# Kernel tuning notes

Measured on AMD Instinct MI355X. Metric: run time of the kernel, lower is better.

## Reference

```python
import jax, jax.numpy as jnp
import numpy as np
import math

D_MODEL = 1024
N_HEADS = 16
HEAD_DIM = D_MODEL // N_HEADS
TEMP = 0.1          # sinkhorn temperature
SINK_ITERS = 10     # update_permutation uses n_iterations=10
EPS = 1e-10


def setup_inputs() -> dict:
    key = jax.random.key(0)
    ks = jax.random.split(key, 16)
    b, n, d = 2, 2048, D_MODEL
    x_data = jax.random.normal(ks[0], (b, n, d), dtype=jnp.float32)
    certainty = jax.random.uniform(ks[1], (b, n), dtype=jnp.float32)
    permutation = jnp.stack([jax.random.permutation(jax.random.fold_in(ks[2], i), n)
                             for i in range(b)]).astype(jnp.int64)
    def lin(k):
        kw, kb = jax.random.split(k)
        W = jax.random.normal(kw, (d, d), dtype=jnp.float32) * 0.02
        bvec = jax.random.normal(kb, (d,), dtype=jnp.float32) * 0.02
        return W, bvec
    Wq, bq = lin(ks[3]); Wk, bk = lin(ks[4]); Wv, bv = lin(ks[5]); Wo, bo = lin(ks[6])
    perm_bias_scale = jnp.ones((1, N_HEADS, 1, 1), dtype=jnp.float32)
    certainty_temp = jnp.ones((1,), dtype=jnp.float32) * 2.0
    return {"x_data": x_data, "certainty": certainty, "permutation": permutation,
            "Wq": Wq, "bq": bq, "Wk": Wk, "bk": bk, "Wv": Wv, "bv": bv,
            "Wo": Wo, "bo": bo, "perm_bias_scale": perm_bias_scale,
            "certainty_temp": certainty_temp}


def reference(x_data, certainty, permutation, Wq, bq, Wk, bk, Wv, bv, Wo, bo,
              perm_bias_scale, certainty_temp):
    b, n, d = x_data.shape
    scale = math.sqrt(HEAD_DIM)

    def proj(W, bias):  # nn.Linear: x @ W.T + b, then split heads -> (b,H,n,hd)
        y = jnp.einsum('bnd,ed->bne', x_data, W) + bias
        return y.reshape(b, n, N_HEADS, HEAD_DIM).transpose(0, 2, 1, 3)

    Q, K, V = proj(Wq, bq), proj(Wk, bk), proj(Wv, bv)

    scores = jnp.einsum('bhnk,bhmk->bhnm', Q, K) / scale  # (b,H,n,n)
    # permutation-distance bias: B[i,j] = -|sigma(i)-sigma(j)| * |scale_h|
    pf = permutation.astype(jnp.float32)
    dist = jnp.abs(pf[:, :, None] - pf[:, None, :])       # (b,n,n)
    scores = scores - dist[:, None, :, :] * jnp.abs(perm_bias_scale)

    attention = jax.nn.softmax(scores, axis=-1)           # dropout is identity (eval)
    out = jnp.einsum('bhnm,bhmd->bhnd', attention, V)
    out = out.transpose(0, 2, 1, 3).reshape(b, n, d)
    output = jnp.einsum('bnd,ed->bne', out, Wo) + bo

    # certainty update from attention entropy
    ent = -(attention * jnp.log(attention + EPS)).sum(-1).mean(1)  # (b,n)
    cert_upd = jax.nn.sigmoid(certainty_temp * (math.log(n) - ent))
    new_certainty = jnp.maximum(certainty, cert_upd)

    # permutation update via Sinkhorn on log mean attention
    avg_attn = attention.mean(axis=1)
    P = jnp.exp(jnp.log(avg_attn + EPS) / TEMP)
    def body(_, P):
        P = P / (P.sum(-1, keepdims=True) + EPS)
        P = P / (P.sum(-2, keepdims=True) + EPS)
        return P
    P = jax.lax.fori_loop(0, SINK_ITERS, body, P)
    idx = jnp.argmax(P, axis=-1)                          # (b,n)
    new_permutation = jnp.take_along_axis(permutation, idx, axis=1)

    return output, new_certainty, new_permutation
```

## Files before the change

### kernel.cpp

```cpp
#include <hip/hip_runtime.h>
#include <cstdint>

#define NTOK 2048
#define DMODEL 1024
#define NHEADS 16
#define HD 64
#define BATCH 2
#define EPSF 1e-10f
#define EPSD 1e-10

typedef __attribute__((ext_vector_type(8))) short bf16x8;
typedef __attribute__((ext_vector_type(8))) _Float16 f16x8;
typedef __attribute__((ext_vector_type(4))) float f32x4;

__device__ __forceinline__ float bf2f(unsigned short u){
  union { unsigned int i; float f; } c; c.i = ((unsigned int)u) << 16; return c.f;
}
__device__ __forceinline__ unsigned short f2bf(float f){
  union { float f; unsigned int u; } c; c.f = f;
  unsigned int u = c.u;
  unsigned int r = (u + 0x7FFFu + ((u >> 16) & 1u)) >> 16;
  return (unsigned short)r;
}
__device__ __forceinline__ unsigned short f2h(float f){
  union { _Float16 h; unsigned short u; } c; c.h = (_Float16)f; return c.u;
}
__device__ __forceinline__ float h2f(unsigned short u){
  union { unsigned short u; _Float16 h; } c; c.u = u; return (float)c.h;
}

__device__ __forceinline__ void async16(const unsigned short* g, unsigned short* lds_base){
  __builtin_amdgcn_global_load_lds((const __attribute__((address_space(1))) unsigned int*)g,
                                   (__attribute__((address_space(3))) unsigned int*)lds_base,
                                   16, 0, 0);
}

template<int BM, int BN>
__device__ __forceinline__ void gemm_bt_core(
    const unsigned short* A, int lda,
    const unsigned short* B, int ldb,
    int K,
    f32x4 (&acc)[BM/32][BN/32],
    unsigned short* ldsA, unsigned short* ldsB)
{
  constexpr int TM = BM/32, TN = BN/32;
  const int tid  = threadIdx.x;
  const int lane = tid & 63;
  const int wave = tid >> 6;
  const int wm = wave >> 1, wn = wave & 1;
  const int fr = lane & 15;
  const int fk = (lane >> 4) << 3;
  const int sr = lane >> 2;
  const int sk = (lane & 3) << 3;

  for (int k0 = 0; k0 < K; k0 += 32){
    #pragma unroll
    for (int c = 0; c < BM/64; c++){
      int ch = c*4 + wave;
      async16(A + (long)(ch*16 + sr)*lda + (k0 + sk), ldsA + ch*512);
    }
    #pragma unroll
    for (int c = 0; c < BN/64; c++){
      int ch = c*4 + wave;
      async16(B + (long)(ch*16 + sr)*ldb + (k0 + sk), ldsB + ch*512);
    }
    __syncthreads();
    bf16x8 af[TM], bf[TN];
    #pragma unroll
    for (int i=0;i<TM;i++)
      af[i] = *(const bf16x8*)(ldsA + ((wm*TM*16) + i*16 + fr)*32 + fk);
    #pragma unroll
    for (int j=0;j<TN;j++)
      bf[j] = *(const bf16x8*)(ldsB + ((wn*TN*16) + j*16 + fr)*32 + fk);
    #pragma unroll
    for (int i=0;i<TM;i++)
      #pragma unroll
      for (int j=0;j<TN;j++)
        acc[i][j] = __builtin_amdgcn_mfma_f32_16x16x32_bf16(af[i], bf[j], acc[i][j], 0, 0, 0);
    __syncthreads();
  }
}

__device__ __forceinline__ double wred_sumd(double x){
  for(int o=32;o;o>>=1) x+=__shfl_xor(x,o); return x;
}


__global__ void f2b_multi(const float* __restrict__ x,
    const float* __restrict__ wq, const float* __restrict__ wk,
    const float* __restrict__ wv, const float* __restrict__ wo,
    unsigned short* __restrict__ out)
{
  int i = blockIdx.x*256 + threadIdx.x;
  int base = i << 2;
  const float* src;
  if (base < 4194304) src = x + base;
  else {
    int d = base - 4194304;
    int r = d >> 20, off = d & 1048575;
    src = (r==0 ? wq : (r==1 ? wk : (r==2 ? wv : wo))) + off;
  }
  float4 v = *(const float4*)src;
  ushort4 o;
  o.x = f2bf(v.x); o.y = f2bf(v.y); o.z = f2bf(v.z); o.w = f2bf(v.w);
  *(ushort4*)(out + base) = o;
}

__global__ void init_kernel(double* __restrict__ uv){
  int idx = blockIdx.x*256 + threadIdx.x;
  if (idx < 8192) uv[idx] = 1.0;
}

__global__ __launch_bounds__(256) void qkv_kernel(
    const unsigned short* __restrict__ xb,
    const unsigned short* __restrict__ Wqb, const float* __restrict__ bq,
    const unsigned short* __restrict__ Wkb, const float* __restrict__ bk,
    const unsigned short* __restrict__ Wvb, const float* __restrict__ bv,
    unsigned short* __restrict__ Qb, unsigned short* __restrict__ Kb,
    unsigned short* __restrict__ Vb)
{
  __shared__ unsigned short lds[(128+128)*32];
  int sel = blockIdx.y >> 3;
  int n0 = (blockIdx.y & 7) * 128;
  int m0 = blockIdx.x * 128;
  const unsigned short* W = sel==0 ? Wqb : (sel==1 ? Wkb : Wvb);
  const float* bias       = sel==0 ? bq  : (sel==1 ? bk  : bv);
  unsigned short* out     = sel==0 ? Qb  : (sel==1 ? Kb  : Vb);
  f32x4 acc[4][4];
  f32x4 z = {0.f,0.f,0.f,0.f};
  for (int i=0;i<4;i++) for(int j=0;j<4;j++) acc[i][j] = z;
  gemm_bt_core<128,128>(xb + (long)m0*DMODEL, DMODEL, W + (long)n0*DMODEL, DMODEL,
                        DMODEL, acc, lds, lds + 128*32);
  int lane = threadIdx.x & 63, wave = threadIdx.x >> 6;
  int wm = wave>>1, wn = wave&1;
  int cr = (lane>>4)<<2, cc = lane & 15;
  for (int i=0;i<4;i++) for(int j=0;j<4;j++) for(int r=0;r<4;r++){
    int row = m0 + wm*64 + i*16 + cr + r;
    int col = n0 + wn*64 + j*16 + cc;
    out[(long)row*DMODEL + col] = f2bf(acc[i][j][r] + bias[col]);
  }
}

__global__ void vtrans_kernel(const unsigned short* __restrict__ Vb,
                              unsigned short* __restrict__ Vt)
{
  __shared__ unsigned short t[32][33];
  int b = blockIdx.z, i0 = blockIdx.x*32, e0 = blockIdx.y*32;
  int tx = threadIdx.x, ty = threadIdx.y;
  for (int r=0;r<32;r+=8) t[ty+r][tx] = Vb[((long)b*NTOK + i0+ty+r)*DMODEL + e0+tx];
  __syncthreads();
  for (int r=0;r<32;r+=8)
    Vt[((long)b*DMODEL + e0+ty+r)*NTOK + i0+tx] = f2h(bf2f(t[tx][ty+r]));
}

__global__ __launch_bounds__(512,4) void attnA_kernel(
    const unsigned short* __restrict__ Qb, const unsigned short* __restrict__ Kb,
    const unsigned short* __restrict__ Vt, const int* __restrict__ perm,
    const float* __restrict__ psc,
    float* __restrict__ mpart, float* __restrict__ lpart, float* __restrict__ Tpart,
    unsigned short* __restrict__ Opart)
{
  __shared__ unsigned short Kt[2*128*32];
  __shared__ unsigned short Vtl[64*136];
  __shared__ unsigned short Pt[128*136];
  __shared__ unsigned short pbs[2048];

  const int tid  = threadIdx.x;
  const int lane = tid & 63;
  const int wave = tid >> 6;
  const int fr   = lane & 15;
  const int fkg  = lane >> 4;
  const int fk   = fkg << 3;
  const int cr   = fkg << 2;
  const int rw   = wave << 4;
  const int rt   = blockIdx.x >> 1;
  const int half = blockIdx.x & 1;
  const int m0   = rt * 128;
  const int h    = blockIdx.y;
  const int b    = blockIdx.z;

  for (int i = tid; i < 2048; i += 512) pbs[i] = (unsigned short)perm[b*NTOK + i];

  bf16x8 qf[2];
  #pragma unroll
  for (int kc=0;kc<2;kc++)
    qf[kc] = *(const bf16x8*)(Qb + ((long)(b*NTOK + m0 + rw + fr))*DMODEL + h*HD + kc*32 + fk);

  const float asc = fabsf(psc[h]);
  __syncthreads();

  float prow[4];
  #pragma unroll
  for (int r=0;r<4;r++) prow[r] = (float)pbs[m0 + rw + cr + r];

  float mrow[4], lrow[4], Trow[4];
  #pragma unroll
  for (int r=0;r<4;r++){ mrow[r] = -1e30f; lrow[r] = 0.f; Trow[r] = 0.f; }
  f32x4 oacc[4];
  {
    f32x4 z = {0.f,0.f,0.f,0.f};
    for (int jj=0;jj<4;jj++) oacc[jj]=z;
  }

  for (int j2=0;j2<8;j2++){
    int j = half*8 + j2;
    __syncthreads();
    #pragma unroll
    for (int c=0;c<2;c++){
      int q = c*8 + wave;
      int kc = q >> 3, rb = (q & 7) * 16;
      async16(Kb + ((long)(b*NTOK + j*128 + rb + (lane>>2)))*DMODEL + h*HD + kc*32 + ((lane&3)<<3),
              Kt + kc*4096 + rb*32);
    }
    {
      int c = tid>>3, sg = tid&7;
      const unsigned short* vg = Vt + ((long)(b*DMODEL + h*HD + c))*NTOK + j*128 + sg*16;
      unsigned short* vl = Vtl + c*136 + sg*16;
      *(uint4*)(vl)   = *(const uint4*)(vg);
      *(uint4*)(vl+8) = *(const uint4*)(vg+8);
    }
    __syncthreads();

    f32x4 sacc[8];
    {
      f32x4 z = {0.f,0.f,0.f,0.f};
      for (int jj=0;jj<8;jj++) sacc[jj]=z;
    }
    #pragma unroll
    for (int kc=0;kc<2;kc++){
      bf16x8 bfr[8];
      #pragma unroll
      for (int jj=0;jj<8;jj++) bfr[jj] = *(const bf16x8*)(Kt + kc*4096 + (jj*16+fr)*32 + fk);
      #pragma unroll
      for (int jj=0;jj<8;jj++)
        sacc[jj] = __builtin_amdgcn_mfma_f32_16x16x32_bf16(qf[kc], bfr[jj], sacc[jj],0,0,0);
    }

    float pcol[8];
    #pragma unroll
    for (int jj=0;jj<8;jj++) pcol[jj] = (float)pbs[j*128 + jj*16 + fr];

    #pragma unroll
    for (int r=0;r<4;r++){
      float sv[8];
      float tm = -1e30f;
      #pragma unroll
      for (int jj=0;jj<8;jj++){
        sv[jj] = sacc[jj][r]*0.125f - fabsf(prow[r]-pcol[jj])*asc;
        tm = fmaxf(tm, sv[jj]);
      }
      #pragma unroll
      for (int o=1;o<16;o<<=1) tm = fmaxf(tm, __shfl_xor(tm,o));
      float nm = fmaxf(mrow[r], tm);
      float alpha = __expf(mrow[r] - nm);
      float lres = lrow[r]*alpha;
      Trow[r] = Trow[r]*alpha + (mrow[r]-nm)*lres;
      #pragma unroll
      for (int jc=0;jc<4;jc++) oacc[jc][r] *= alpha;
      float ts=0.f, tT=0.f;
      int prowbase = (rw + cr + r)*136;
      #pragma unroll
      for (int jj=0;jj<8;jj++){
        float d = sv[jj]-nm;
        float ev = __expf(d);
        ts += ev; tT += ev*d;
        Pt[prowbase + jj*16 + fr] = f2h(ev);
      }
      #pragma unroll
      for (int o=1;o<16;o<<=1){ ts += __shfl_xor(ts,o); tT += __shfl_xor(tT,o); }
      lrow[r] = lres + ts;
      Trow[r] += tT;
      mrow[r] = nm;
    }
    __syncthreads();
    #pragma unroll
    for (int kp=0;kp<4;kp++){
      f16x8 paf, pbf[4];
      paf = *(const f16x8*)(Pt + (rw+fr)*136 + kp*32 + fk);
      #pragma unroll
      for (int jj=0;jj<4;jj++) pbf[jj] = *(const f16x8*)(Vtl + (jj*16+fr)*136 + kp*32 + fk);
      #pragma unroll
      for (int jj=0;jj<4;jj++)
        oacc[jj] = __builtin_amdgcn_mfma_f32_16x16x32_f16(paf, pbf[jj], oacc[jj],0,0,0);
    }
  }

  long pbase = ((long)(half*BATCH + b)*NHEADS + h)*NTOK;
  #pragma unroll
  for (int jj=0;jj<4;jj++)
    #pragma unroll
    for (int r=0;r<4;r++){
      int row = m0 + rw + cr + r;
      Opart[(pbase + row)*HD + jj*16 + fr] = f2bf(oacc[jj][r]);
    }
  if (fr == 0){
    #pragma unroll
    for (int r=0;r<4;r++){
      int row = m0 + rw + cr + r;
      mpart[pbase + row] = mrow[r];
      lpart[pbase + row] = lrow[r];
      Tpart[pbase + row] = Trow[r];
    }
  }
}

__global__ __launch_bounds__(256) void merge_kernel(
    const float* __restrict__ mpart, const float* __restrict__ lpart,
    const float* __restrict__ Tpart, const unsigned short* __restrict__ Opart,
    unsigned short* __restrict__ Ob, float* __restrict__ mbuf,
    float* __restrict__ ilbuf, float* __restrict__ entb)
{
  int tid = threadIdx.x;
  int row = blockIdx.x*4 + (tid>>6);
  int h = blockIdx.y;
  int b = blockIdx.z;
  int col = tid & 63;
  long o1 = ((long)(0*BATCH + b)*NHEADS + h)*NTOK + row;
  long o2 = ((long)(1*BATCH + b)*NHEADS + h)*NTOK + row;
  float m1 = mpart[o1], m2 = mpart[o2];
  float l1 = lpart[o1], l2 = lpart[o2];
  float m = fmaxf(m1, m2);
  float e1 = __expf(m1-m), e2 = __expf(m2-m);
  float l = l1*e1 + l2*e2;
  float il = 1.0f/l;
  float Ov = (bf2f(Opart[o1*HD + col])*e1 + bf2f(Opart[o2*HD + col])*e2)*il;
  Ob[((long)(b*NTOK + row))*DMODEL + h*HD + col] = f2bf(Ov);
  if (col == 0){
    float T = e1*(Tpart[o1] + (m1-m)*l1) + e2*(Tpart[o2] + (m2-m)*l2);
    long off = ((long)(b*NHEADS+h))*NTOK + row;
    mbuf[off] = m; ilbuf[off] = il;
    entb[off] = T*il - __logf(l);
  }
}

__global__ __launch_bounds__(512,4) void avgP_kernel(
    const unsigned short* __restrict__ Qb, const unsigned short* __restrict__ Kb,
    const int* __restrict__ perm, const float* __restrict__ psc,
    const float* __restrict__ mbuf, const float* __restrict__ ilbuf,
    float* __restrict__ avg, unsigned short* __restrict__ avgH,
    unsigned short* __restrict__ avgT)
{
  __shared__ unsigned short Kt[2][8192];
  __shared__ float sm[NHEADS*64];
  __shared__ float si[NHEADS*64];
  __shared__ float sasc[NHEADS];

  const int bid = blockIdx.x;
  const int xcd = bid & 7, idx = bid >> 3;
  const int b   = xcd >> 2;
  const int qy  = (xcd >> 1) & 1, qx = xcd & 1;
  const int ydim = qy*16 + (idx >> 3);
  const int xdim = qx*8  + (idx & 7);
  const int m0   = ydim * 64;
  const int colb = xdim * 128;

  const int tid  = threadIdx.x;
  const int lane = tid & 63;
  const int wave = tid >> 6;
  const int wr = wave >> 2, wc = wave & 3;
  const int rw = wr*32, cb = wc*32;
  const int fr = lane & 15;
  const int fk = (lane >> 4) << 3;
  const int cr = (lane >> 4) << 2;
  const int cc = lane & 15;
  const int sr = lane >> 2;
  const int sk = (lane & 3) << 3;

  const unsigned short* kgp[2];
  int ldsoff[2];
  #pragma unroll
  for (int q=0;q<2;q++){
    int cid = q*8 + wave;
    int kc = cid >> 3, ch = cid & 7;
    kgp[q] = Kb + ((long)(b*NTOK + colb + ch*16 + sr))*DMODEL + kc*32 + sk;
    ldsoff[q] = kc*4096 + ch*512;
  }

  for (int e = tid; e < NHEADS*64; e += 512){
    int h = e >> 6, r = e & 63;
    long off = ((long)(b*NHEADS + h))*NTOK + m0 + r;
    sm[e] = mbuf[off];
    si[e] = ilbuf[off];
  }
  if (tid < NHEADS) sasc[tid] = fabsf(psc[tid]);

  float prw[8];
  #pragma unroll
  for (int i=0;i<2;i++)
    #pragma unroll
    for (int r=0;r<4;r++)
      prw[i*4+r] = (float)perm[b*NTOK + m0 + rw + i*16 + cr + r];
  float pcl[2];
  #pragma unroll
  for (int j=0;j<2;j++)
    pcl[j] = (float)perm[b*NTOK + colb + cb + j*16 + cc];

  const unsigned short* qp[2];
  #pragma unroll
  for (int i=0;i<2;i++)
    qp[i] = Qb + ((long)(b*NTOK + m0 + rw + i*16 + fr))*DMODEL + fk;

  float aacc[2][2][4];
  #pragma unroll
  for (int i=0;i<2;i++) for (int j=0;j<2;j++) for (int r=0;r<4;r++) aacc[i][j][r]=0.f;

  #pragma unroll
  for (int q=0;q<2;q++) async16(kgp[q], &Kt[0][0] + ldsoff[q]);
  __syncthreads();

  unsigned short* curb = &Kt[0][0];
  unsigned short* nxtb = &Kt[1][0];

  #pragma unroll 2
  for (int h=0; h<NHEADS; h++){
    if (h < NHEADS-1){
      #pragma unroll
      for (int q=0;q<2;q++) async16(kgp[q] + (h+1)*HD, nxtb + ldsoff[q]);
    }
    bf16x8 qf[2][2];
    #pragma unroll
    for (int i=0;i<2;i++)
      #pragma unroll
      for (int kc=0;kc<2;kc++)
        qf[i][kc] = *(const bf16x8*)(qp[i] + h*HD + kc*32);

    f32x4 acc[2][2];
    {
      f32x4 z = {0.f,0.f,0.f,0.f};
      acc[0][0]=z; acc[0][1]=z; acc[1][0]=z; acc[1][1]=z;
    }
    #pragma unroll
    for (int kc=0;kc<2;kc++){
      bf16x8 bfr[2];
      #pragma unroll
      for (int j=0;j<2;j++)
        bfr[j] = *(const bf16x8*)(curb + kc*4096 + ((cb>>4) + j)*512 + fr*32 + fk);
      #pragma unroll
      for (int i=0;i<2;i++)
        #pragma unroll
        for (int j=0;j<2;j++)
          acc[i][j] = __builtin_amdgcn_mfma_f32_16x16x32_bf16(qf[i][kc], bfr[j], acc[i][j],0,0,0);
    }
    const float asc = sasc[h];
    #pragma unroll
    for (int i=0;i<2;i++)
      #pragma unroll
      for (int r=0;r<4;r++){
        int rl = rw + i*16 + cr + r;
        float mh = sm[h*64 + rl];
        float ih = si[h*64 + rl];
        #pragma unroll
        for (int j=0;j<2;j++){
          float sv = acc[i][j][r]*0.125f - fabsf(prw[i*4+r]-pcl[j])*asc;
          aacc[i][j][r] += __expf(sv - mh) * ih;
        }
      }
    __syncthreads();
    unsigned short* t = curb; curb = nxtb; nxtb = t;
  }

  unsigned short* T = &Kt[0][0];
  #pragma unroll
  for (int i=0;i<2;i++)
    #pragma unroll
    for (int j=0;j<2;j++)
      #pragma unroll
      for (int r=0;r<4;r++){
        float pw = __expf(__logf(aacc[i][j][r]*0.0625f + EPSF)*10.0f);
        int rl = rw + i*16 + cr + r;
        int cl = cb + j*16 + cc;
        long off = ((long)(b*NTOK + m0 + rl))*NTOK + colb + cl;
        avg[off] = pw;
        unsigned short hv = f2h(pw);
        avgH[off] = hv;
        T[cl*72 + rl] = hv;
      }
  __syncthreads();
  {
    int c = tid >> 2, sg = tid & 3;
    uint4* dst = (uint4*)(avgT + ((long)(b*NTOK + colb + c))*NTOK + m0 + sg*16);
    const unsigned short* src = T + c*72 + sg*16;
    dst[0] = *(const uint4*)(src);
    dst[1] = *(const uint4*)(src + 8);
  }
}

__global__ __launch_bounds__(256) void sink_phase_h(const unsigned short* __restrict__ M,
    const double* __restrict__ x, double* __restrict__ y)
{
  int b = blockIdx.y, tid = threadIdx.x;
  int wave = tid >> 6, lane = tid & 63;
  int i = blockIdx.x*4 + wave;
  const unsigned short* row = M + ((long)b*NTOK + i)*NTOK;
  const double* xb = x + b*NTOK;
  double s = 0.0;
  #pragma unroll
  for (int k=0;k<4;k++){
    int j = k*512 + lane*8;
    f16x8 mv = *(const f16x8*)(row + j);
    #pragma unroll
    for (int e=0;e<8;e++) s += (double)(float)mv[e] * xb[j+e];
  }
  s = wred_sumd(s);
  if (lane == 0){
    double yi = y[b*NTOK + i];
    y[b*NTOK + i] = yi / (yi*s + EPSD);
  }
}

__global__ __launch_bounds__(256) void argmax_kernel(const float* __restrict__ P,
    const double* __restrict__ v, const int* __restrict__ perm,
    float* __restrict__ dout_perm)
{
  int b = blockIdx.y, tid = threadIdx.x;
  int wave = tid >> 6, lane = tid & 63;
  int i = blockIdx.x*4 + wave;
  const float* row = P + ((long)b*NTOK + i)*NTOK;
  const double* vb = v + b*NTOK;
  double bv = -1.0; int bj = 0;
  #pragma unroll
  for (int k=0;k<4;k++){
    int j0 = k*512 + lane*8;
    float4 r0 = *(const float4*)(row + j0);
    float4 r1 = *(const float4*)(row + j0 + 4);
    float rv[8] = {r0.x,r0.y,r0.z,r0.w,r1.x,r1.y,r1.z,r1.w};
    #pragma unroll
    for (int e=0;e<8;e++){
      double val = (double)rv[e]*vb[j0+e];
      if (val>bv){ bv=val; bj=j0+e; }
    }
  }
  for (int o=32;o;o>>=1){
    double ov=__shfl_xor(bv,o); int oj=__shfl_xor(bj,o);
    if (ov>bv || (ov==bv && oj<bj)){bv=ov;bj=oj;}
  }
  if (lane == 0)
    dout_perm[b*NTOK + i] = (float)perm[b*NTOK + bj];
}

__global__ __launch_bounds__(256) void out_kernel(
    const unsigned short* __restrict__ Ob, const unsigned short* __restrict__ Wob,
    const float* __restrict__ bo, float* __restrict__ dout)
{
  __shared__ unsigned short lds[(128+128)*32];
  int m0 = blockIdx.x*128, n0 = blockIdx.y*128;
  f32x4 acc[4][4];
  f32x4 z = {0.f,0.f,0.f,0.f};
  for (int i=0;i<4;i++) for(int j=0;j<4;j++) acc[i][j] = z;
  gemm_bt_core<128,128>(Ob + (long)m0*DMODEL, DMODEL, Wob + (long)n0*DMODEL, DMODEL,
                        DMODEL, acc, lds, lds + 128*32);
  int lane = threadIdx.x & 63, wave = threadIdx.x >> 6;
  int wm = wave>>1, wn = wave&1;
  int cr = (lane>>4)<<2, cc = lane & 15;
  for (int i=0;i<4;i++) for(int j=0;j<4;j++) for(int r=0;r<4;r++){
    int row = m0 + wm*64 + i*16 + cr + r;
    int col = n0 + wn*64 + j*16 + cc;
    dout[(long)row*DMODEL + col] = acc[i][j][r] + bo[col];
  }
}

__global__ void cert_kernel(const float* __restrict__ cert,
    const float* __restrict__ ctemp, const float* __restrict__ entb,
    float* __restrict__ dout_cert)
{
  int idx = blockIdx.x*256+threadIdx.x;
  if (idx >= BATCH*NTOK) return;
  int b = idx >> 11, row = idx & 2047;
  float s = 0.f;
  #pragma unroll
  for (int h=0; h<NHEADS; h++) s += entb[((long)(b*NHEADS+h))*NTOK + row];
  float ent = -s * (1.0f/16.0f);
  float ct = ctemp[0];
  float arg = ct * (logf((float)NTOK) - ent);
  float upd = 1.0f/(1.0f+expf(-arg));
  dout_cert[idx] = fmaxf(cert[idx], upd);
}

extern "C" void kernel_launch(void* const* d_in, const int* in_sizes, int n_in,
                              void* d_out, int out_size, void* d_ws, size_t ws_size,
                              hipStream_t stream)
{
  const float* x    = (const float*)d_in[0];
  const float* cert = (const float*)d_in[1];
  const int*   perm = (const int*)d_in[2];
  const float* Wq   = (const float*)d_in[3];
  const float* bq   = (const float*)d_in[4];
  const float* Wk   = (const float*)d_in[5];
  const float* bk   = (const float*)d_in[6];
  const float* Wv   = (const float*)d_in[7];
  const float* bv   = (const float*)d_in[8];
  const float* Wo   = (const float*)d_in[9];
  const float* bo   = (const float*)d_in[10];
  const float* psc  = (const float*)d_in[11];
  const float* ctmp = (const float*)d_in[12];
  float* dout = (float*)d_out;

  double* u    = (double*)d_ws;
  double* v    = u + 4096;
  float* avg   = (float*)(v + 4096);
  float* mbuf  = avg   + 8388608;
  float* ilbuf = mbuf  + 65536;
  float* entb  = ilbuf + 65536;
  float* mpart = entb  + 65536;
  float* lpart = mpart + 131072;
  float* Tpart = lpart + 131072;
  unsigned short* Opart = (unsigned short*)(Tpart + 131072);
  unsigned short* xb  = Opart + 8388608;
  unsigned short* Wqb = xb  + 4194304;
  unsigned short* Wkb = Wqb + 1048576;
  unsigned short* Wvb = Wkb + 1048576;
  unsigned short* Wob = Wvb + 1048576;
  unsigned short* Qb  = Wob + 1048576;
  unsigned short* Kb  = Qb  + 4194304;
  unsigned short* Vb  = Kb  + 4194304;
  unsigned short* Vt  = Vb  + 4194304;
  unsigned short* Ob  = Vt  + 4194304;
  unsigned short* avgH = Opart;
  unsigned short* avgT = Vb;

  f2b_multi<<<dim3(8192),256,0,stream>>>(x, Wq, Wk, Wv, Wo, xb);
  init_kernel<<<dim3(32),256,0,stream>>>(u);

  qkv_kernel<<<dim3(32,24),256,0,stream>>>(xb, Wqb,bq, Wkb,bk, Wvb,bv, Qb,Kb,Vb);
  vtrans_kernel<<<dim3(64,32,2), dim3(32,8),0,stream>>>(Vb, Vt);

  attnA_kernel<<<dim3(32,NHEADS,2),512,0,stream>>>(Qb, Kb, Vt, perm, psc,
      mpart, lpart, Tpart, Opart);
  merge_kernel<<<dim3(512,NHEADS,2),256,0,stream>>>(mpart, lpart, Tpart, Opart,
      Ob, mbuf, ilbuf, entb);
  avgP_kernel<<<dim3(1024),512,0,stream>>>(Qb, Kb, perm, psc, mbuf, ilbuf,
      avg, avgH, avgT);

  for (int it=0; it<10; it++){
    sink_phase_h<<<dim3(512,2),256,0,stream>>>(avgH, v, u);
    sink_phase_h<<<dim3(512,2),256,0,stream>>>(avgT, u, v);
  }
  argmax_kernel<<<dim3(512,2),256,0,stream>>>(avg, v, perm, dout + 4194304 + 4096);

  out_kernel <<<dim3(32,8),256,0,stream>>>(Ob, Wob, bo, dout);
  cert_kernel<<<dim3(16), 256,0,stream>>>(cert, ctmp, entb, dout + 4194304);
}
```

Measured before the change: 498.4 us.

## Fuse Sinkhorn iterations into persistent grid-barrier kernel; lazy softmax rescale; repad LDS

Replaces the 20 separate Sinkhorn launches plus the init and argmax kernels with one persistent kernel of 256 blocks that synchronises through an atomic grid barrier, which removes launch overhead and per-launch tails. In the attention kernel, the running max is only updated when the new tile max exceeds it by more than a threshold, which skips the rescale work on most tiles. The LDS row padding also changes from 136 to 132. The grid barrier assumes all 256 blocks are co-resident, so it can deadlock if they are not, and the lazy rescale lets exponentials reach larger values before overflow-safe rescaling.

```diff
diff --git a/kernel.cpp b/kernel.cpp
--- a/kernel.cpp
+++ b/kernel.cpp
@@ -85,6 +85,28 @@
   for(int o=32;o;o>>=1) x+=__shfl_xor(x,o); return x;
 }
 
+__device__ __forceinline__ void gridbar(unsigned int* bar){
+  __syncthreads();
+  if (threadIdx.x == 0){
+    __threadfence();
+    unsigned int g = __hip_atomic_load(bar+1, __ATOMIC_RELAXED, __HIP_MEMORY_SCOPE_AGENT);
+    unsigned int a = __hip_atomic_fetch_add(bar, 1u, __ATOMIC_ACQ_REL, __HIP_MEMORY_SCOPE_AGENT);
+    if (a == 255u){
+      __hip_atomic_store(bar,   0u,  __ATOMIC_RELAXED, __HIP_MEMORY_SCOPE_AGENT);
+      __hip_atomic_store(bar+1, g+1u, __ATOMIC_RELEASE, __HIP_MEMORY_SCOPE_AGENT);
+    } else {
+      while (__hip_atomic_load(bar+1, __ATOMIC_ACQUIRE, __HIP_MEMORY_SCOPE_AGENT) == g)
+        __builtin_amdgcn_s_sleep(32);
+    }
+    __threadfence();
+  }
+  __syncthreads();
+}
+
+
+__global__ void barinit_kernel(unsigned int* __restrict__ bar){
+  if (threadIdx.x == 0){ bar[0] = 0u; bar[1] = 0u; }
+}
 
 __global__ void f2b_multi(const float* __restrict__ x,
     const float* __restrict__ wq, const float* __restrict__ wk,
@@ -104,11 +126,6 @@
   ushort4 o;
   o.x = f2bf(v.x); o.y = f2bf(v.y); o.z = f2bf(v.z); o.w = f2bf(v.w);
   *(ushort4*)(out + base) = o;
-}
-
-__global__ void init_kernel(double* __restrict__ uv){
-  int idx = blockIdx.x*256 + threadIdx.x;
-  if (idx < 8192) uv[idx] = 1.0;
 }
 
 __global__ __launch_bounds__(256) void qkv_kernel(
@@ -161,8 +178,8 @@
     unsigned short* __restrict__ Opart)
 {
   __shared__ unsigned short Kt[2*128*32];
-  __shared__ unsigned short Vtl[64*136];
-  __shared__ unsigned short Pt[128*136];
+  __shared__ unsigned short Vtl[64*132];
+  __shared__ unsigned short Pt[128*132];
   __shared__ unsigned short pbs[2048];
 
   const int tid  = threadIdx.x;
@@ -215,7 +232,7 @@
     {
       int c = tid>>3, sg = tid&7;
       const unsigned short* vg = Vt + ((long)(b*DMODEL + h*HD + c))*NTOK + j*128 + sg*16;
-      unsigned short* vl = Vtl + c*136 + sg*16;
+      unsigned short* vl = Vtl + c*132 + sg*16;
       *(uint4*)(vl)   = *(const uint4*)(vg);
       *(uint4*)(vl+8) = *(const uint4*)(vg+8);
     }
@@ -251,34 +268,36 @@
       }
       #pragma unroll
       for (int o=1;o<16;o<<=1) tm = fmaxf(tm, __shfl_xor(tm,o));
-      float nm = fmaxf(mrow[r], tm);
-      float alpha = __expf(mrow[r] - nm);
-      float lres = lrow[r]*alpha;
-      Trow[r] = Trow[r]*alpha + (mrow[r]-nm)*lres;
-      #pragma unroll
-      for (int jc=0;jc<4;jc++) oacc[jc][r] *= alpha;
+      float d0 = tm - mrow[r];
+      if (d0 > 8.0f){
+        float al = __expf(-d0);
+        #pragma unroll
+        for (int jc=0;jc<4;jc++) oacc[jc][r] *= al;
+        Trow[r] = Trow[r]*al - d0*(lrow[r]*al);
+        lrow[r] *= al;
+        mrow[r] = tm;
+      }
       float ts=0.f, tT=0.f;
-      int prowbase = (rw + cr + r)*136;
+      int prowbase = (rw + cr + r)*132;
       #pragma unroll
       for (int jj=0;jj<8;jj++){
-        float d = sv[jj]-nm;
+        float d = sv[jj]-mrow[r];
         float ev = __expf(d);
         ts += ev; tT += ev*d;
         Pt[prowbase + jj*16 + fr] = f2h(ev);
       }
       #pragma unroll
       for (int o=1;o<16;o<<=1){ ts += __shfl_xor(ts,o); tT += __shfl_xor(tT,o); }
-      lrow[r] = lres + ts;
+      lrow[r] += ts;
       Trow[r] += tT;
-      mrow[r] = nm;
     }
     __syncthreads();
     #pragma unroll
     for (int kp=0;kp<4;kp++){
       f16x8 paf, pbf[4];
-      paf = *(const f16x8*)(Pt + (rw+fr)*136 + kp*32 + fk);
-      #pragma unroll
-      for (int jj=0;jj<4;jj++) pbf[jj] = *(const f16x8*)(Vtl + (jj*16+fr)*136 + kp*32 + fk);
+      paf = *(const f16x8*)(Pt + (rw+fr)*132 + kp*32 + fk);
+      #pragma unroll
+      for (int jj=0;jj<4;jj++) pbf[jj] = *(const f16x8*)(Vtl + (jj*16+fr)*132 + kp*32 + fk);
       #pragma unroll
       for (int jj=0;jj<4;jj++)
         oacc[jj] = __builtin_amdgcn_mfma_f32_16x16x32_f16(paf, pbf[jj], oacc[jj],0,0,0);
@@ -485,44 +504,56 @@
   }
 }
 
-__global__ __launch_bounds__(256) void sink_phase_h(const unsigned short* __restrict__ M,
-    const double* __restrict__ x, double* __restrict__ y)
-{
-  int b = blockIdx.y, tid = threadIdx.x;
-  int wave = tid >> 6, lane = tid & 63;
-  int i = blockIdx.x*4 + wave;
-  const unsigned short* row = M + ((long)b*NTOK + i)*NTOK;
-  const double* xb = x + b*NTOK;
-  double s = 0.0;
-  #pragma unroll
-  for (int k=0;k<4;k++){
-    int j = k*512 + lane*8;
-    f16x8 mv = *(const f16x8*)(row + j);
-    #pragma unroll
-    for (int e=0;e<8;e++) s += (double)(float)mv[e] * xb[j+e];
-  }
-  s = wred_sumd(s);
-  if (lane == 0){
-    double yi = y[b*NTOK + i];
-    y[b*NTOK + i] = yi / (yi*s + EPSD);
-  }
-}
-
-__global__ __launch_bounds__(256) void argmax_kernel(const float* __restrict__ P,
-    const double* __restrict__ v, const int* __restrict__ perm,
-    float* __restrict__ dout_perm)
-{
-  int b = blockIdx.y, tid = threadIdx.x;
-  int wave = tid >> 6, lane = tid & 63;
-  int i = blockIdx.x*4 + wave;
-  const float* row = P + ((long)b*NTOK + i)*NTOK;
-  const double* vb = v + b*NTOK;
+__global__ __launch_bounds__(1024,4) void sink_persist(
+    const unsigned short* __restrict__ MH, const unsigned short* __restrict__ MT,
+    double* __restrict__ u, double* __restrict__ v,
+    const float* __restrict__ P, const int* __restrict__ perm,
+    float* __restrict__ dout_perm, unsigned int* __restrict__ bar)
+{
+  const int tid  = threadIdx.x;
+  const int wave = tid >> 6, lane = tid & 63;
+  const int row  = blockIdx.x*16 + wave;
+  const int b    = row >> 11, i = row & 2047;
+  const unsigned short* rowH = MH + ((long)(b*NTOK) + i)*NTOK;
+  const unsigned short* rowT = MT + ((long)(b*NTOK) + i)*NTOK;
+  double* ub = u + b*NTOK;
+  double* vb = v + b*NTOK;
+
+  if (lane == 0){ ub[i] = 1.0; vb[i] = 1.0; }
+  gridbar(bar);
+
+  for (int it=0; it<10; it++){
+    double s = 0.0;
+    #pragma unroll
+    for (int k=0;k<4;k++){
+      int j = k*512 + lane*8;
+      f16x8 mv = *(const f16x8*)(rowH + j);
+      #pragma unroll
+      for (int e=0;e<8;e++) s += (double)(float)mv[e] * vb[j+e];
+    }
+    s = wred_sumd(s);
+    if (lane == 0){ double ui = ub[i]; ub[i] = ui / (ui*s + EPSD); }
+    gridbar(bar);
+    s = 0.0;
+    #pragma unroll
+    for (int k=0;k<4;k++){
+      int j = k*512 + lane*8;
+      f16x8 mv = *(const f16x8*)(rowT + j);
+      #pragma unroll
+      for (int e=0;e<8;e++) s += (double)(float)mv[e] * ub[j+e];
+    }
+    s = wred_sumd(s);
+    if (lane == 0){ double vi = vb[i]; vb[i] = vi / (vi*s + EPSD); }
+    gridbar(bar);
+  }
+
+  const float* rowP = P + ((long)(b*NTOK) + i)*NTOK;
   double bv = -1.0; int bj = 0;
   #pragma unroll
   for (int k=0;k<4;k++){
     int j0 = k*512 + lane*8;
-    float4 r0 = *(const float4*)(row + j0);
-    float4 r1 = *(const float4*)(row + j0 + 4);
+    float4 r0 = *(const float4*)(rowP + j0);
+    float4 r1 = *(const float4*)(rowP + j0 + 4);
     float rv[8] = {r0.x,r0.y,r0.z,r0.w,r1.x,r1.y,r1.z,r1.w};
     #pragma unroll
     for (int e=0;e<8;e++){
@@ -615,11 +646,12 @@
   unsigned short* Vb  = Kb  + 4194304;
   unsigned short* Vt  = Vb  + 4194304;
   unsigned short* Ob  = Vt  + 4194304;
+  unsigned int* bar   = (unsigned int*)(Ob + 4194304);
   unsigned short* avgH = Opart;
   unsigned short* avgT = Vb;
 
+  barinit_kernel<<<dim3(1),64,0,stream>>>(bar);
   f2b_multi<<<dim3(8192),256,0,stream>>>(x, Wq, Wk, Wv, Wo, xb);
-  init_kernel<<<dim3(32),256,0,stream>>>(u);
 
   qkv_kernel<<<dim3(32,24),256,0,stream>>>(xb, Wqb,bq, Wkb,bk, Wvb,bv, Qb,Kb,Vb);
   vtrans_kernel<<<dim3(64,32,2), dim3(32,8),0,stream>>>(Vb, Vt);
@@ -631,11 +663,8 @@
   avgP_kernel<<<dim3(1024),512,0,stream>>>(Qb, Kb, perm, psc, mbuf, ilbuf,
       avg, avgH, avgT);
 
-  for (int it=0; it<10; it++){
-    sink_phase_h<<<dim3(512,2),256,0,stream>>>(avgH, v, u);
-    sink_phase_h<<<dim3(512,2),256,0,stream>>>(avgT, u, v);
-  }
-  argmax_kernel<<<dim3(512,2),256,0,stream>>>(avg, v, perm, dout + 4194304 + 4096);
+  sink_persist<<<dim3(256),1024,0,stream>>>(avgH, avgT, u, v, avg, perm,
+      dout + 4194304 + 4096, bar);
 
   out_kernel <<<dim3(32,8),256,0,stream>>>(Ob, Wob, bo, dout);
   cert_kernel<<<dim3(16), 256,0,stream>>>(cert, ctmp, entb, dout + 4194304);
```

Result: slower. 1.327 ms (+166.2%).
